# Optimization experiments

Hardware: AMD Instinct MI355X
Metric: run time of the kernel (lower is better)

The kernel has to match this reference:

```python
import jax, jax.numpy as jnp
import numpy as np

N = 50000
E = 800000
F_IN = 256
H = 64      # hidden_channels
NH = 4      # GAT heads

def setup_inputs() -> dict:
    key = jax.random.key(0)
    ks = jax.random.split(key, 16)
    x = jax.random.normal(ks[0], (N, F_IN), dtype=jnp.float32)
    edge_index = jax.random.randint(ks[1], (2, E), 0, N, dtype=jnp.int64)
    def w(k, shape, fan_in):
        return jax.random.normal(k, shape, dtype=jnp.float32) / np.sqrt(fan_in)
    return {
        "x": x, "edge_index": edge_index,
        "W1": w(ks[2], (F_IN, H), F_IN), "b1": jnp.zeros((H,), jnp.float32),
        "W2": w(ks[3], (H, H), H),       "b2": jnp.zeros((H,), jnp.float32),
        "Wg": w(ks[4], (H, NH * H), H),
        "att_src": w(ks[5], (NH, H), H), "att_dst": w(ks[6], (NH, H), H),
        "bg": jnp.zeros((NH * H,), jnp.float32),
        "Wf1": w(ks[7], (NH * H, H), NH * H), "bf1": jnp.zeros((H,), jnp.float32),
        "Wf2": w(ks[8], (H, 1), H),           "bf2": jnp.zeros((1,), jnp.float32),
    }

def _with_self_loops(edge_index):
    loops = jnp.arange(N, dtype=edge_index.dtype)
    src = jnp.concatenate([edge_index[0], loops])
    dst = jnp.concatenate([edge_index[1], loops])
    return src, dst

def _gcn(h, src, dst, W, b):
    # h: [N, d_in] -> [N, d_out]; symmetric norm D^-1/2 (A+I) D^-1/2
    h = h @ W
    deg = jax.ops.segment_sum(jnp.ones_like(dst, dtype=h.dtype), dst, num_segments=N)
    dinv = jnp.where(deg > 0, jax.lax.rsqrt(deg), 0.0)
    norm = dinv[src] * dinv[dst]                      # [E2]
    out = jax.ops.segment_sum(h[src] * norm[:, None], dst, num_segments=N)
    return out + b

def _gat(h, src, dst, Wg, att_src, att_dst, bg):
    hp = (h @ Wg).reshape(N, NH, H)                   # [N, NH, H]
    a_src = jnp.einsum('nhd,hd->nh', hp, att_src)     # [N, NH]
    a_dst = jnp.einsum('nhd,hd->nh', hp, att_dst)
    alpha = jax.nn.leaky_relu(a_src[src] + a_dst[dst], negative_slope=0.2)  # [E2, NH]
    amax = jax.ops.segment_max(alpha, dst, num_segments=N)
    e = jnp.exp(alpha - amax[dst])
    denom = jax.ops.segment_sum(e, dst, num_segments=N)
    coef = e / denom[dst]                             # [E2, NH]
    out = jax.ops.segment_sum(hp[src] * coef[:, :, None], dst, num_segments=N)
    return out.reshape(N, NH * H) + bg

def reference(x, edge_index, W1, b1, W2, b2, Wg, att_src, att_dst, bg, Wf1, bf1, Wf2, bf2):
    src, dst = _with_self_loops(edge_index)
    h = jax.nn.relu(_gcn(x, src, dst, W1, b1))        # dropout inactive (eval)
    h = jax.nn.relu(_gcn(h, src, dst, W2, b2))
    h = _gat(h, src, dst, Wg, att_src, att_dst, bg)
    h = jax.nn.relu(h @ Wf1 + bf1)
    return h @ Wf2 + bf2                              # [N, 1]
```

## Files before the change

kernel.cpp:

```cpp
#include <hip/hip_runtime.h>
#include <hip/hip_fp16.h>
#include <math.h>


#define CAP 64
#define CAPSH 6

typedef _Float16 v4h __attribute__((ext_vector_type(4)));
typedef float v4f __attribute__((ext_vector_type(4)));

__device__ __forceinline__ float lrelu02(float a) { return fmaxf(a, 0.2f * a); }

__device__ __forceinline__ float4 lrelu4(float4 a) {
    return make_float4(lrelu02(a.x), lrelu02(a.y), lrelu02(a.z), lrelu02(a.w));
}

__device__ __forceinline__ float4 exp4(float4 a) {
    return make_float4(__expf(a.x), __expf(a.y), __expf(a.z), __expf(a.w));
}

__device__ __forceinline__ float4 unpack4(float2 raw) {
    __half2 h01 = *(__half2*)&raw.x;
    __half2 h23 = *(__half2*)&raw.y;
    float2 f01 = __half22float2(h01);
    float2 f23 = __half22float2(h23);
    return make_float4(f01.x, f01.y, f23.x, f23.y);
}

__device__ __forceinline__ float2 pack4(float4 v) {
    float2 r;
    *(__half2*)&r.x = __float22half2_rn(make_float2(v.x, v.y));
    *(__half2*)&r.y = __float22half2_rn(make_float2(v.z, v.w));
    return r;
}


#define GEMM_BODY(BX, K, COLS)                                                     \
    __shared__ float As[16][68];                                                   \
    __shared__ float Bs[16][64];                                                   \
    const int row0 = (BX) * 64;                                                    \
    const int col0 = blockIdx.y * 64;                                              \
    const int t = threadIdx.x;                                                     \
    const int tx = t & 15;                                                         \
    const int ty = t >> 4;                                                         \
    const int lm = t >> 2;                                                         \
    const int lk4 = (t & 3) << 2;                                                  \
    const int wk = t >> 4;                                                         \
    const int wc = (t & 15) << 2;                                                  \
    float acc[4][4] = {};                                                          \
    for (int k0 = 0; k0 < K; k0 += 16) {                                           \
        float4 av = make_float4(0.f, 0.f, 0.f, 0.f);                               \
        int r = row0 + lm;                                                         \
        if (r < nrows) av = *(const float4*)(X + (size_t)r * K + k0 + lk4);        \
        As[lk4 + 0][lm] = av.x;                                                    \
        As[lk4 + 1][lm] = av.y;                                                    \
        As[lk4 + 2][lm] = av.z;                                                    \
        As[lk4 + 3][lm] = av.w;                                                    \
        *(float4*)&Bs[wk][wc] = *(const float4*)(W + (size_t)(k0 + wk) * COLS + col0 + wc); \
        __syncthreads();                                                           \
        _Pragma("unroll") for (int kk = 0; kk < 16; kk++) {                        \
            float4 a = *(const float4*)&As[kk][ty << 2];                           \
            float4 b = *(const float4*)&Bs[kk][tx << 2];                           \
            acc[0][0] = fmaf(a.x, b.x, acc[0][0]);                                 \
            acc[0][1] = fmaf(a.x, b.y, acc[0][1]);                                 \
            acc[0][2] = fmaf(a.x, b.z, acc[0][2]);                                 \
            acc[0][3] = fmaf(a.x, b.w, acc[0][3]);                                 \
            acc[1][0] = fmaf(a.y, b.x, acc[1][0]);                                 \
            acc[1][1] = fmaf(a.y, b.y, acc[1][1]);                                 \
            acc[1][2] = fmaf(a.y, b.z, acc[1][2]);                                 \
            acc[1][3] = fmaf(a.y, b.w, acc[1][3]);                                 \
            acc[2][0] = fmaf(a.z, b.x, acc[2][0]);                                 \
            acc[2][1] = fmaf(a.z, b.y, acc[2][1]);                                 \
            acc[2][2] = fmaf(a.z, b.z, acc[2][2]);                                 \
            acc[2][3] = fmaf(a.z, b.w, acc[2][3]);                                 \
            acc[3][0] = fmaf(a.w, b.x, acc[3][0]);                                 \
            acc[3][1] = fmaf(a.w, b.y, acc[3][1]);                                 \
            acc[3][2] = fmaf(a.w, b.z, acc[3][2]);                                 \
            acc[3][3] = fmaf(a.w, b.w, acc[3][3]);                                 \
        }                                                                          \
        __syncthreads();                                                           \
    }

__launch_bounds__(256)
__global__ void k_fused1(const int* __restrict__ src, const int* __restrict__ dst, int E,
                         int* __restrict__ cnt, unsigned short* __restrict__ slots,
                         const float* __restrict__ X, const float* __restrict__ W,
                         __half* __restrict__ Y, int nrows, int gemmBlocks,
                         const float* __restrict__ Wg, const float* __restrict__ att_src,
                         const float* __restrict__ att_dst, const float* __restrict__ Wf1,
                         const float* __restrict__ bf1, const float* __restrict__ bg,
                         const float* __restrict__ W2, float* __restrict__ watt,
                         __half* __restrict__ WcF, __half* __restrict__ W2F,
                         float* __restrict__ bias2) {
    if ((int)blockIdx.x >= gemmBlocks) {
        int b2 = blockIdx.x - gemmBlocks;
        int tt = threadIdx.x;
        if (b2 < 64) {
            int idx = b2 * 256 + tt;
            int r = idx >> 6, c = idx & 63;
            int h = r >> 6, k = r & 63;
            float s = 0.f;
            for (int j = 0; j < 64; j++)
                s = fmaf(Wg[k * 256 + h * 64 + j], Wf1[(h * 64 + j) * 64 + c], s);
            int ks = r >> 4, kr = r & 15;
            int lfrag = ((kr >> 2) << 4) | (c & 15);
            int jf = kr & 3;
            int w = c >> 4;
            WcF[((((w << 4) | ks) << 6) | lfrag) * 4 + jf] = __float2half_rn(s);
        } else if (b2 == 64) {
            for (int idx = tt; idx < 512; idx += 256) {
                int k = idx >> 3, c8 = idx & 7;
                int h = c8 & 3;
                const float* att = (c8 < 4) ? att_src : att_dst;
                float s = 0.f;
                for (int c = 0; c < 64; c++)
                    s = fmaf(Wg[k * 256 + h * 64 + c], att[h * 64 + c], s);
                watt[k * 8 + c8] = s;
            }
            if (tt < 64) {
                float s = bf1[tt];
                for (int j = 0; j < 256; j++) s = fmaf(bg[j], Wf1[j * 64 + tt], s);
                bias2[tt] = s;
            }
            for (int f = tt; f < 4096; f += 256) {
                int jf = f & 3, lfrag = (f >> 2) & 63, ws = f >> 8;
                int w = ws >> 2, ks = ws & 3;
                int k = ks * 16 + ((lfrag >> 4) << 2) + jf;
                int c = w * 16 + (lfrag & 15);
                W2F[f] = __float2half_rn(W2[k * 64 + c]);
            }
        } else {
            int e = (b2 - 65) * 256 + tt;
            if (e < E) {
                int d = dst[e];
                int p = atomicAdd(&cnt[d], 1);
                if (p < CAP) slots[((size_t)d << CAPSH) + p] = (unsigned short)src[e];
            }
        }
        return;
    }
    GEMM_BODY(blockIdx.x, 256, 64)
#pragma unroll
    for (int i = 0; i < 4; i++) {
        int row = row0 + (ty << 2) + i;
        if (row >= nrows) break;
        float4 o = make_float4(acc[i][0], acc[i][1], acc[i][2], acc[i][3]);
        ((float2*)(Y + (size_t)row * 64))[tx] = pack4(o);
    }
}


__launch_bounds__(256)
__global__ void k_gcn1_gemm2(const __half* __restrict__ A, const unsigned short* __restrict__ slots,
                             const int* __restrict__ cnt, const float* __restrict__ b1,
                             const __half* __restrict__ W2F, __half* __restrict__ A2, int n) {
    __shared__ alignas(16) __half s_oh[16 * 68];
    __shared__ alignas(16) __half s_res[16 * 68];
    __shared__ float s_dv[16];
    int t = threadIdx.x;
    int lane = t & 63;
    int l = t & 15;
    int nb = t >> 4;
    int v = blockIdx.x * 16 + nb;
    bool act = (v < n);
    if (act) {
        int deg = min(cnt[v], CAP);
        const unsigned short* lst = slots + ((size_t)v << CAPSH);
        float dv = rsqrtf((float)(deg + 1));
        float4 a0 = unpack4(((const float2*)(A + (size_t)v * 64))[l]);
        a0.x *= dv; a0.y *= dv; a0.z *= dv; a0.w *= dv;
        float4 a1 = make_float4(0.f, 0.f, 0.f, 0.f);
        float4 a2 = a1, a3 = a1;
        int j = 0;
        for (; j + 3 < deg; j += 4) {
            ushort4 s4 = *(const ushort4*)(lst + j);
            float c0 = rsqrtf((float)(cnt[s4.x] + 1));
            float c1 = rsqrtf((float)(cnt[s4.y] + 1));
            float c2 = rsqrtf((float)(cnt[s4.z] + 1));
            float c3 = rsqrtf((float)(cnt[s4.w] + 1));
            float4 t0 = unpack4(((const float2*)(A + (size_t)s4.x * 64))[l]);
            float4 t1 = unpack4(((const float2*)(A + (size_t)s4.y * 64))[l]);
            float4 t2 = unpack4(((const float2*)(A + (size_t)s4.z * 64))[l]);
            float4 t3 = unpack4(((const float2*)(A + (size_t)s4.w * 64))[l]);
            a0.x = fmaf(c0, t0.x, a0.x); a0.y = fmaf(c0, t0.y, a0.y);
            a0.z = fmaf(c0, t0.z, a0.z); a0.w = fmaf(c0, t0.w, a0.w);
            a1.x = fmaf(c1, t1.x, a1.x); a1.y = fmaf(c1, t1.y, a1.y);
            a1.z = fmaf(c1, t1.z, a1.z); a1.w = fmaf(c1, t1.w, a1.w);
            a2.x = fmaf(c2, t2.x, a2.x); a2.y = fmaf(c2, t2.y, a2.y);
            a2.z = fmaf(c2, t2.z, a2.z); a2.w = fmaf(c2, t2.w, a2.w);
            a3.x = fmaf(c3, t3.x, a3.x); a3.y = fmaf(c3, t3.y, a3.y);
            a3.z = fmaf(c3, t3.z, a3.z); a3.w = fmaf(c3, t3.w, a3.w);
        }
        for (; j < deg; j++) {
            int sa = lst[j];
            float ca = rsqrtf((float)(cnt[sa] + 1));
            float4 ta = unpack4(((const float2*)(A + (size_t)sa * 64))[l]);
            a0.x = fmaf(ca, ta.x, a0.x); a0.y = fmaf(ca, ta.y, a0.y);
            a0.z = fmaf(ca, ta.z, a0.z); a0.w = fmaf(ca, ta.w, a0.w);
        }
        a0.x += a1.x + a2.x + a3.x;
        a0.y += a1.y + a2.y + a3.y;
        a0.z += a1.z + a2.z + a3.z;
        a0.w += a1.w + a2.w + a3.w;
        float4 b = ((const float4*)b1)[l];
        float4 o;
        o.x = fmaxf(fmaf(dv, a0.x, b.x), 0.f);
        o.y = fmaxf(fmaf(dv, a0.y, b.y), 0.f);
        o.z = fmaxf(fmaf(dv, a0.z, b.z), 0.f);
        o.w = fmaxf(fmaf(dv, a0.w, b.w), 0.f);
        *(float2*)&s_oh[nb * 68 + (l << 2)] = pack4(o);
        if (l == 0) s_dv[nb] = dv;
    } else {
        *(float2*)&s_oh[nb * 68 + (l << 2)] = make_float2(0.f, 0.f);
        if (l == 0) s_dv[nb] = 0.f;
    }
    __syncthreads();
    int w = t >> 6;
    v4f acc = {0.f, 0.f, 0.f, 0.f};
    int arow = (lane & 15) * 68;
    int acol = (lane >> 4) << 2;
#pragma unroll
    for (int ks = 0; ks < 4; ks++) {
        v4h a = *(const v4h*)&s_oh[arow + ks * 16 + acol];
        v4h bfr = *(const v4h*)&W2F[((((w << 2) | ks) << 6) | lane) << 2];
        acc = __builtin_amdgcn_mfma_f32_16x16x16f16(a, bfr, acc, 0, 0, 0);
    }
    int cc = (w << 4) | (lane & 15);
    int m0 = (lane >> 4) << 2;
#pragma unroll
    for (int j = 0; j < 4; j++)
        s_res[(m0 + j) * 68 + cc] = __float2half_rn(acc[j] * s_dv[m0 + j]);
    __syncthreads();
    if (act)
        ((float2*)(A2 + (size_t)v * 64))[l] = *(const float2*)&s_res[nb * 68 + (l << 2)];
}


__launch_bounds__(256)
__global__ void k_gcn2_att(const __half* __restrict__ T, const unsigned short* __restrict__ slots,
                           const int* __restrict__ cnt, const float* __restrict__ bias,
                           const float* __restrict__ watt, __half* __restrict__ Out,
                           float* __restrict__ asrc, float* __restrict__ adst, int n) {
    int t = threadIdx.x;
    int l = t & 15;
    int v = blockIdx.x * 16 + (t >> 4);
    if (v >= n) return;
    int deg = min(cnt[v], CAP);
    const unsigned short* lst = slots + ((size_t)v << CAPSH);
    float dv = rsqrtf((float)(deg + 1));
    float4 a0 = unpack4(((const float2*)(T + (size_t)v * 64))[l]);
    float4 a1 = make_float4(0.f, 0.f, 0.f, 0.f);
    float4 a2 = a1, a3 = a1;
    int j = 0;
    for (; j + 3 < deg; j += 4) {
        ushort4 s4 = *(const ushort4*)(lst + j);
        float4 t0 = unpack4(((const float2*)(T + (size_t)s4.x * 64))[l]);
        float4 t1 = unpack4(((const float2*)(T + (size_t)s4.y * 64))[l]);
        float4 t2 = unpack4(((const float2*)(T + (size_t)s4.z * 64))[l]);
        float4 t3 = unpack4(((const float2*)(T + (size_t)s4.w * 64))[l]);
        a0.x += t0.x; a0.y += t0.y; a0.z += t0.z; a0.w += t0.w;
        a1.x += t1.x; a1.y += t1.y; a1.z += t1.z; a1.w += t1.w;
        a2.x += t2.x; a2.y += t2.y; a2.z += t2.z; a2.w += t2.w;
        a3.x += t3.x; a3.y += t3.y; a3.z += t3.z; a3.w += t3.w;
    }
    for (; j < deg; j++) {
        float4 ta = unpack4(((const float2*)(T + (size_t)lst[j] * 64))[l]);
        a0.x += ta.x; a0.y += ta.y; a0.z += ta.z; a0.w += ta.w;
    }
    a0.x += a1.x + a2.x + a3.x;
    a0.y += a1.y + a2.y + a3.y;
    a0.z += a1.z + a2.z + a3.z;
    a0.w += a1.w + a2.w + a3.w;
    float4 b = ((const float4*)bias)[l];
    float4 o;
    o.x = fmaxf(fmaf(dv, a0.x, b.x), 0.f);
    o.y = fmaxf(fmaf(dv, a0.y, b.y), 0.f);
    o.z = fmaxf(fmaf(dv, a0.z, b.z), 0.f);
    o.w = fmaxf(fmaf(dv, a0.w, b.w), 0.f);
    ((float2*)(Out + (size_t)v * 64))[l] = pack4(o);
    const float* wr = watt + (l << 2) * 8;
    float4 w0a = *(const float4*)(wr +  0), w0b = *(const float4*)(wr +  4);
    float4 w1a = *(const float4*)(wr +  8), w1b = *(const float4*)(wr + 12);
    float4 w2a = *(const float4*)(wr + 16), w2b = *(const float4*)(wr + 20);
    float4 w3a = *(const float4*)(wr + 24), w3b = *(const float4*)(wr + 28);
    float4 ds, dd;
    ds.x = o.x*w0a.x + o.y*w1a.x + o.z*w2a.x + o.w*w3a.x;
    ds.y = o.x*w0a.y + o.y*w1a.y + o.z*w2a.y + o.w*w3a.y;
    ds.z = o.x*w0a.z + o.y*w1a.z + o.z*w2a.z + o.w*w3a.z;
    ds.w = o.x*w0a.w + o.y*w1a.w + o.z*w2a.w + o.w*w3a.w;
    dd.x = o.x*w0b.x + o.y*w1b.x + o.z*w2b.x + o.w*w3b.x;
    dd.y = o.x*w0b.y + o.y*w1b.y + o.z*w2b.y + o.w*w3b.y;
    dd.z = o.x*w0b.z + o.y*w1b.z + o.z*w2b.z + o.w*w3b.z;
    dd.w = o.x*w0b.w + o.y*w1b.w + o.z*w2b.w + o.w*w3b.w;
    for (int off = 1; off <= 8; off <<= 1) {
        ds.x += __shfl_xor(ds.x, off); ds.y += __shfl_xor(ds.y, off);
        ds.z += __shfl_xor(ds.z, off); ds.w += __shfl_xor(ds.w, off);
        dd.x += __shfl_xor(dd.x, off); dd.y += __shfl_xor(dd.y, off);
        dd.z += __shfl_xor(dd.z, off); dd.w += __shfl_xor(dd.w, off);
    }
    if (l == 0) {
        ((float4*)asrc)[v] = ds;
        ((float4*)adst)[v] = dd;
    }
}


__launch_bounds__(256)
__global__ void k_gat_head(const __half* __restrict__ Bt, const unsigned short* __restrict__ slots,
                           const int* __restrict__ cnt, const float* __restrict__ asrc,
                           const float* __restrict__ adst, const __half* __restrict__ WcF,
                           const float* __restrict__ bias2, const float* __restrict__ Wf2,
                           const float* __restrict__ bf2, float* __restrict__ out, int n) {
    __shared__ alignas(16) __half s_aggh[16 * 260];
    __shared__ alignas(16) float s_e[16 * 68];
    __shared__ int s_sidx[16 * 17];
    __shared__ float s_part[16][4];
    int t = threadIdx.x;
    int lane = t & 63;
    int l = lane & 15;
    int nb = t >> 4;
    int v = blockIdx.x * 16 + nb;
    bool act = (v < n);
    if (act) {
        int deg = min(cnt[v], CAP);
        const unsigned short* lst = slots + ((size_t)v << CAPSH);
        float4 ad4 = ((const float4*)adst)[v];
        float4 as4 = ((const float4*)asrc)[v];
        float4 es = exp4(lrelu4(make_float4(as4.x + ad4.x, as4.y + ad4.y,
                                            as4.z + ad4.z, as4.w + ad4.w)));
        float4 esum = (l == 0) ? es : make_float4(0.f, 0.f, 0.f, 0.f);
        float4 bv = unpack4(((const float2*)(Bt + (size_t)v * 64))[l]);
        float4 acc0 = make_float4(es.x * bv.x, es.x * bv.y, es.x * bv.z, es.x * bv.w);
        float4 acc1 = make_float4(es.y * bv.x, es.y * bv.y, es.y * bv.z, es.y * bv.w);
        float4 acc2 = make_float4(es.z * bv.x, es.z * bv.y, es.z * bv.z, es.z * bv.w);
        float4 acc3 = make_float4(es.w * bv.x, es.w * bv.y, es.w * bv.z, es.w * bv.w);
        for (int c0 = 0; c0 < deg; c0 += 16) {
            int cl = min(16, deg - c0);
            float4 e = make_float4(0.f, 0.f, 0.f, 0.f);
            if (l < cl) {
                int s = lst[c0 + l];
                float4 sa = ((const float4*)asrc)[s];
                e = exp4(lrelu4(make_float4(sa.x + ad4.x, sa.y + ad4.y,
                                            sa.z + ad4.z, sa.w + ad4.w)));
                esum.x += e.x; esum.y += e.y; esum.z += e.z; esum.w += e.w;
                s_sidx[nb * 17 + l] = s;
            }
            *(float4*)&s_e[nb * 68 + (l << 2)] = e;
            __builtin_amdgcn_sched_barrier(0);
            for (int jj = 0; jj < cl; jj++) {
                int so = s_sidx[nb * 17 + jj];
                float4 ev = *(const float4*)&s_e[nb * 68 + (jj << 2)];
                float4 tv = unpack4(((const float2*)(Bt + (size_t)so * 64))[l]);
                acc0.x = fmaf(ev.x, tv.x, acc0.x); acc0.y = fmaf(ev.x, tv.y, acc0.y);
                acc0.z = fmaf(ev.x, tv.z, acc0.z); acc0.w = fmaf(ev.x, tv.w, acc0.w);
                acc1.x = fmaf(ev.y, tv.x, acc1.x); acc1.y = fmaf(ev.y, tv.y, acc1.y);
                acc1.z = fmaf(ev.y, tv.z, acc1.z); acc1.w = fmaf(ev.y, tv.w, acc1.w);
                acc2.x = fmaf(ev.z, tv.x, acc2.x); acc2.y = fmaf(ev.z, tv.y, acc2.y);
                acc2.z = fmaf(ev.z, tv.z, acc2.z); acc2.w = fmaf(ev.z, tv.w, acc2.w);
                acc3.x = fmaf(ev.w, tv.x, acc3.x); acc3.y = fmaf(ev.w, tv.y, acc3.y);
                acc3.z = fmaf(ev.w, tv.z, acc3.z); acc3.w = fmaf(ev.w, tv.w, acc3.w);
            }
        }
        for (int o = 8; o >= 1; o >>= 1) {
            esum.x += __shfl_xor(esum.x, o); esum.y += __shfl_xor(esum.y, o);
            esum.z += __shfl_xor(esum.z, o); esum.w += __shfl_xor(esum.w, o);
        }
        float i0 = 1.f / esum.x, i1 = 1.f / esum.y, i2 = 1.f / esum.z, i3 = 1.f / esum.w;
        *(float2*)&s_aggh[nb * 260 +   0 + (l << 2)] =
            pack4(make_float4(acc0.x*i0, acc0.y*i0, acc0.z*i0, acc0.w*i0));
        *(float2*)&s_aggh[nb * 260 +  64 + (l << 2)] =
            pack4(make_float4(acc1.x*i1, acc1.y*i1, acc1.z*i1, acc1.w*i1));
        *(float2*)&s_aggh[nb * 260 + 128 + (l << 2)] =
            pack4(make_float4(acc2.x*i2, acc2.y*i2, acc2.z*i2, acc2.w*i2));
        *(float2*)&s_aggh[nb * 260 + 192 + (l << 2)] =
            pack4(make_float4(acc3.x*i3, acc3.y*i3, acc3.z*i3, acc3.w*i3));
    } else {
        float2 z = make_float2(0.f, 0.f);
        *(float2*)&s_aggh[nb * 260 +   0 + (l << 2)] = z;
        *(float2*)&s_aggh[nb * 260 +  64 + (l << 2)] = z;
        *(float2*)&s_aggh[nb * 260 + 128 + (l << 2)] = z;
        *(float2*)&s_aggh[nb * 260 + 192 + (l << 2)] = z;
    }
    __syncthreads();
    int w = t >> 6;
    v4f accA = {0.f, 0.f, 0.f, 0.f};
    v4f accB = {0.f, 0.f, 0.f, 0.f};
    int arow = l * 260;
    int acol = (lane >> 4) << 2;
#pragma unroll
    for (int ks = 0; ks < 16; ks += 2) {
        v4h a0f = *(const v4h*)&s_aggh[arow + ks * 16 + acol];
        v4h b0f = *(const v4h*)&WcF[((((w << 4) | ks) << 6) | lane) << 2];
        accA = __builtin_amdgcn_mfma_f32_16x16x16f16(a0f, b0f, accA, 0, 0, 0);
        v4h a1f = *(const v4h*)&s_aggh[arow + (ks + 1) * 16 + acol];
        v4h b1f = *(const v4h*)&WcF[((((w << 4) | (ks + 1)) << 6) | lane) << 2];
        accB = __builtin_amdgcn_mfma_f32_16x16x16f16(a1f, b1f, accB, 0, 0, 0);
    }
    int cc = (w << 4) | l;
    float bb = bias2[cc], wq = Wf2[cc];
    float p0 = fmaxf(accA[0] + accB[0] + bb, 0.f) * wq;
    float p1 = fmaxf(accA[1] + accB[1] + bb, 0.f) * wq;
    float p2 = fmaxf(accA[2] + accB[2] + bb, 0.f) * wq;
    float p3 = fmaxf(accA[3] + accB[3] + bb, 0.f) * wq;
    for (int o = 1; o <= 8; o <<= 1) {
        p0 += __shfl_xor(p0, o); p1 += __shfl_xor(p1, o);
        p2 += __shfl_xor(p2, o); p3 += __shfl_xor(p3, o);
    }
    if (l == 0) {
        int m0 = (lane >> 4) << 2;
        s_part[m0 + 0][w] = p0; s_part[m0 + 1][w] = p1;
        s_part[m0 + 2][w] = p2; s_part[m0 + 3][w] = p3;
    }
    __syncthreads();
    if (t < 16 && blockIdx.x * 16 + t < n)
        out[blockIdx.x * 16 + t] =
            s_part[t][0] + s_part[t][1] + s_part[t][2] + s_part[t][3] + bf2[0];
}


extern "C" void kernel_launch(void* const* d_in, const int* in_sizes, int n_in,
                              void* d_out, int out_size, void* d_ws, size_t ws_size,
                              hipStream_t stream) {
    const float* x       = (const float*)d_in[0];
    const int*   ei      = (const int*)d_in[1];
    const float* W1      = (const float*)d_in[2];
    const float* b1      = (const float*)d_in[3];
    const float* W2      = (const float*)d_in[4];
    const float* b2      = (const float*)d_in[5];
    const float* Wg      = (const float*)d_in[6];
    const float* att_src = (const float*)d_in[7];
    const float* att_dst = (const float*)d_in[8];
    const float* bg      = (const float*)d_in[9];
    const float* Wf1     = (const float*)d_in[10];
    const float* bf1     = (const float*)d_in[11];
    const float* Wf2     = (const float*)d_in[12];
    const float* bf2     = (const float*)d_in[13];
    float* out = (float*)d_out;

    const int N = in_sizes[0] / 256;
    const int E = in_sizes[1] / 2;
    const int* src = ei;
    const int* dst = ei + E;

    char* p = (char*)d_ws;
    auto alloc = [&](size_t bytes) {
        void* r = (void*)p;
        p += (bytes + 255) & ~(size_t)255;
        return r;
    };
    __half* A   = (__half*)alloc((size_t)N * 64 * 2);
    __half* A2  = (__half*)alloc((size_t)N * 64 * 2);
    __half* B   = (__half*)alloc((size_t)N * 64 * 2);
    float* asrc = (float*)alloc((size_t)N * 4 * 4);
    float* adst = (float*)alloc((size_t)N * 4 * 4);
    int*   cnt  = (int*)alloc((size_t)N * 4);
    unsigned short* slots = (unsigned short*)alloc((size_t)N * CAP * 2);
    float* watt   = (float*)alloc(64 * 8 * 4);
    __half* WcF   = (__half*)alloc(256 * 64 * 2);
    __half* W2F   = (__half*)alloc(64 * 64 * 2);
    float* bias2  = (float*)alloc(64 * 4);

    const int gE = (E + 255) / 256;
    const int grow = (N + 63) / 64;
    const int gagg = (N + 15) / 16;

    hipMemsetAsync(cnt, 0, (size_t)N * 4, stream);

    k_fused1<<<grow + 65 + gE, 256, 0, stream>>>(
        src, dst, E, cnt, slots, x, W1, A, N, grow,
        Wg, att_src, att_dst, Wf1, bf1, bg, W2, watt, WcF, W2F, bias2);

    k_gcn1_gemm2<<<gagg, 256, 0, stream>>>(A, slots, cnt, b1, W2F, A2, N);

    k_gcn2_att<<<gagg, 256, 0, stream>>>(A2, slots, cnt, b2, watt, B, asrc, adst, N);

    k_gat_head<<<gagg, 256, 0, stream>>>(B, slots, cnt, asrc, adst,
                                         WcF, bias2, Wf2, bf2, out, N);
}
```

Baseline: 239.2 us.

## Reorder fused kernel blocks: scatter first with 4 edges per thread, pad Bs

Moves the edge-scatter blocks to the front of the fused launch so the latency-bound atomic scatter is dispatched first and overlaps with the GEMM blocks. Each scatter thread now handles four edges, batching the loads and atomics for more memory-level parallelism, and writes slots with nontemporal stores. The B shared tile is also padded to 68 columns to avoid LDS bank conflicts. Block indexing in the GEMM path is shifted to match the new order.

```diff
diff --git a/kernel.cpp b/kernel.cpp
--- a/kernel.cpp
+++ b/kernel.cpp
@@ -37,7 +37,7 @@
 
 #define GEMM_BODY(BX, K, COLS)                                                     \
     __shared__ float As[16][68];                                                   \
-    __shared__ float Bs[16][64];                                                   \
+    __shared__ float Bs[16][68];                                                   \
     const int row0 = (BX) * 64;                                                    \
     const int col0 = blockIdx.y * 64;                                              \
     const int t = threadIdx.x;                                                     \
@@ -85,15 +85,41 @@
 __global__ void k_fused1(const int* __restrict__ src, const int* __restrict__ dst, int E,
                          int* __restrict__ cnt, unsigned short* __restrict__ slots,
                          const float* __restrict__ X, const float* __restrict__ W,
-                         __half* __restrict__ Y, int nrows, int gemmBlocks,
+                         __half* __restrict__ Y, int nrows, int scatBlocks,
                          const float* __restrict__ Wg, const float* __restrict__ att_src,
                          const float* __restrict__ att_dst, const float* __restrict__ Wf1,
                          const float* __restrict__ bf1, const float* __restrict__ bg,
                          const float* __restrict__ W2, float* __restrict__ watt,
                          __half* __restrict__ WcF, __half* __restrict__ W2F,
                          float* __restrict__ bias2) {
-    if ((int)blockIdx.x >= gemmBlocks) {
-        int b2 = blockIdx.x - gemmBlocks;
+    if ((int)blockIdx.x < scatBlocks) {
+        int tt = threadIdx.x;
+        int base = blockIdx.x * 1024 + tt;
+        int e0 = base, e1 = base + 256, e2 = base + 512, e3 = base + 768;
+        int d0 = (e0 < E) ? dst[e0] : 0;
+        int d1 = (e1 < E) ? dst[e1] : 0;
+        int d2 = (e2 < E) ? dst[e2] : 0;
+        int d3 = (e3 < E) ? dst[e3] : 0;
+        int s0 = (e0 < E) ? src[e0] : 0;
+        int s1 = (e1 < E) ? src[e1] : 0;
+        int s2 = (e2 < E) ? src[e2] : 0;
+        int s3 = (e3 < E) ? src[e3] : 0;
+        int p0 = (e0 < E) ? atomicAdd(&cnt[d0], 1) : CAP;
+        int p1 = (e1 < E) ? atomicAdd(&cnt[d1], 1) : CAP;
+        int p2 = (e2 < E) ? atomicAdd(&cnt[d2], 1) : CAP;
+        int p3 = (e3 < E) ? atomicAdd(&cnt[d3], 1) : CAP;
+        if (p0 < CAP) __builtin_nontemporal_store((unsigned short)s0,
+                          &slots[((size_t)d0 << CAPSH) + p0]);
+        if (p1 < CAP) __builtin_nontemporal_store((unsigned short)s1,
+                          &slots[((size_t)d1 << CAPSH) + p1]);
+        if (p2 < CAP) __builtin_nontemporal_store((unsigned short)s2,
+                          &slots[((size_t)d2 << CAPSH) + p2]);
+        if (p3 < CAP) __builtin_nontemporal_store((unsigned short)s3,
+                          &slots[((size_t)d3 << CAPSH) + p3]);
+        return;
+    }
+    if ((int)blockIdx.x < scatBlocks + 65) {
+        int b2 = blockIdx.x - scatBlocks;
         int tt = threadIdx.x;
         if (b2 < 64) {
             int idx = b2 * 256 + tt;
@@ -107,7 +133,7 @@
             int jf = kr & 3;
             int w = c >> 4;
             WcF[((((w << 4) | ks) << 6) | lfrag) * 4 + jf] = __float2half_rn(s);
-        } else if (b2 == 64) {
+        } else {
             for (int idx = tt; idx < 512; idx += 256) {
                 int k = idx >> 3, c8 = idx & 7;
                 int h = c8 & 3;
@@ -129,17 +155,10 @@
                 int c = w * 16 + (lfrag & 15);
                 W2F[f] = __float2half_rn(W2[k * 64 + c]);
             }
-        } else {
-            int e = (b2 - 65) * 256 + tt;
-            if (e < E) {
-                int d = dst[e];
-                int p = atomicAdd(&cnt[d], 1);
-                if (p < CAP) slots[((size_t)d << CAPSH) + p] = (unsigned short)src[e];
-            }
         }
         return;
     }
-    GEMM_BODY(blockIdx.x, 256, 64)
+    GEMM_BODY(blockIdx.x - scatBlocks - 65, 256, 64)
 #pragma unroll
     for (int i = 0; i < 4; i++) {
         int row = row0 + (ty << 2) + i;
@@ -460,14 +479,14 @@
     __half* W2F   = (__half*)alloc(64 * 64 * 2);
     float* bias2  = (float*)alloc(64 * 4);
 
-    const int gE = (E + 255) / 256;
+    const int gScat = (E + 1023) / 1024;
     const int grow = (N + 63) / 64;
     const int gagg = (N + 15) / 16;
 
     hipMemsetAsync(cnt, 0, (size_t)N * 4, stream);
 
-    k_fused1<<<grow + 65 + gE, 256, 0, stream>>>(
-        src, dst, E, cnt, slots, x, W1, A, N, grow,
+    k_fused1<<<gScat + 65 + grow, 256, 0, stream>>>(
+        src, dst, E, cnt, slots, x, W1, A, N, gScat,
         Wg, att_src, att_dst, Wf1, bf1, bg, W2, watt, WcF, W2F, bias2);
 
     k_gcn1_gemm2<<<gagg, 256, 0, stream>>>(A, slots, cnt, b1, W2F, A2, N);
```

After: 271.1 us. 13.3% more time.
